# Optimization experiments

Hardware: AMD Instinct MI355X
Metric: run time of the kernel (lower is better)

Reference implementation:

```python
import jax, jax.numpy as jnp
import numpy as np

SPACE = 63
STRIDE = 2
TEMP = 0.07
W_CHAR, W_WORD, W_PHRASE, W_IDEA = 1.0, 0.5, 0.1, 0.1


def setup_inputs() -> dict:
    key = jax.random.key(0)
    ks = jax.random.split(key, 6)
    B, S, V, D = 8, 4096, 256, 512
    return {
        "logits": jax.random.normal(ks[0], (B, S, V), jnp.float32),
        "word_preds": jax.random.normal(ks[1], (B, D, S // STRIDE), jnp.float32),
        "char_features": jax.random.normal(ks[2], (B, D, S), jnp.float32),
        "contrastive_2": jax.random.normal(ks[3], (B, 128, 1024), jnp.float32),
        "contrastive_3": jax.random.normal(ks[4], (B, 128, 256), jnp.float32),
        "targets": jax.random.randint(ks[5], (B, S), 0, V, jnp.int32),
        "mask": jnp.ones((B, S), jnp.float32),
    }


def _info_nce(emb, temp=TEMP):
    # emb: (B, dim, L). Anchors = even positions, positives = odd positions.
    B, dim, L = emb.shape
    n_pairs = L // 2
    a = emb[:, :, 0:2 * n_pairs:2].transpose(0, 2, 1).reshape(-1, dim)
    p = emb[:, :, 1:2 * n_pairs:2].transpose(0, 2, 1).reshape(-1, dim)
    a = a / jnp.maximum(jnp.linalg.norm(a, axis=1, keepdims=True), 1e-12)
    p = p / jnp.maximum(jnp.linalg.norm(p, axis=1, keepdims=True), 1e-12)
    logits = (a @ p.T) / temp  # (n, n)
    n = logits.shape[0]
    logp = jax.nn.log_softmax(logits, axis=1)
    idx = jnp.arange(n)
    return -jnp.mean(logp[idx, idx])


def _word_span_loss(word_preds, char_features, targets, stride=STRIDE):
    # Segment-mean over spans between consecutive spaces; MSE vs gathered preds.
    B, D, S = char_features.shape
    Wlen = word_preds.shape[2]
    nseg = S + 2  # segment k in [1, n_spaces-1] = span after the k-th space; last slot = junk
    space = targets == SPACE
    cs = jnp.cumsum(space.astype(jnp.int32), axis=1)  # inclusive space count
    seg = jnp.where(space, nseg - 1, cs)          # non-space chars -> span id
    seg_sp = jnp.where(space, cs, nseg - 1)       # space positions -> their space index k
    t_idx = jnp.arange(S, dtype=jnp.int32)

    def per_batch(feats, seg_b, seg_sp_b):
        sums = jax.ops.segment_sum(feats.T, seg_b, num_segments=nseg)  # (nseg, D)
        cnts = jax.ops.segment_sum(jnp.ones((S,), feats.dtype), seg_b, num_segments=nseg)
        pos = jnp.full((nseg,), S, jnp.int32).at[seg_sp_b].set(t_idx)  # position of k-th space
        return sums, cnts, pos

    sums, cnts, pos = jax.vmap(per_batch)(char_features, seg, seg_sp)
    n_sp = cs[:, -1]  # (B,)
    k = jnp.arange(nseg)[None, :]
    valid = (k >= 1) & (k <= n_sp[:, None] - 1) & (cnts > 0) & ((pos // stride) < Wlen)
    means = jax.lax.stop_gradient(sums / jnp.maximum(cnts, 1.0)[..., None])  # target.detach()
    wp = jnp.clip(pos // stride, 0, Wlen - 1)  # (B, nseg)
    preds = jnp.take_along_axis(word_preds.transpose(0, 2, 1), wp[:, :, None], axis=1)  # (B,nseg,D)
    mse = jnp.mean((preds - means) ** 2, axis=-1)  # per-span F.mse_loss (mean over feat dim)
    tot = jnp.sum(jnp.where(valid, mse, 0.0))
    cnt = jnp.sum(valid).astype(mse.dtype)
    return jnp.where(cnt > 0, tot / jnp.maximum(cnt, 1.0), 0.0)


def reference(logits, word_preds, char_features, contrastive_2, contrastive_3, targets, mask):
    # char CE with mask
    logp = jax.nn.log_softmax(logits, axis=-1)
    ce = -jnp.take_along_axis(logp, targets[..., None].astype(jnp.int32), axis=-1)[..., 0]
    n = jnp.sum(mask)
    char_loss = jnp.where(n > 0, jnp.sum(ce * mask) / jnp.maximum(n, 1.0), jnp.mean(ce))
    word_loss = _word_span_loss(word_preds, char_features, targets)
    phrase_loss = _info_nce(contrastive_2)
    idea_loss = _info_nce(contrastive_3)
    return (W_CHAR * char_loss + W_WORD * word_loss
            + W_PHRASE * phrase_loss + W_IDEA * idea_loss)
```

## Files before the change

### kernel.cpp

```cpp
#include <hip/hip_runtime.h>

#define SPACE_TOK 63
#define INV_T 14.285714285714286f
#define SA_SCALE 20.609929155556595f
#define LN2F 0.6931471805599453f

typedef __attribute__((ext_vector_type(8))) short bf16x8;
typedef __attribute__((ext_vector_type(4))) float f32x4;

#define O_CECM   0
#define O_CEM    4096
#define O_CEC    8192
#define O_WPART  12288
#define O_WCNT   14336
#define O_PEXP2  14464
#define O_DIAG2  145536
#define O_PEXP3  161920
#define O_DIAG3  194688
#define O_A2     198848
#define SZ_A2    (4096*128*2)
#define O_P2     (O_A2 + SZ_A2)
#define O_A3     (O_P2 + SZ_A2)
#define SZ_A3    (1024*128*2)
#define O_P3     (O_A3 + SZ_A3)

#define SMEM_A 18048
#define SMEM_B 5632

__device__ inline unsigned short f2bf(float x) {
  union { float f; unsigned int u; } c; c.f = x;
  unsigned int r = c.u + 0x7fffu + ((c.u >> 16) & 1u);
  return (unsigned short)(r >> 16);
}

__device__ void norm_body(char* smem, const float* __restrict__ emb, int L,
                          unsigned short* __restrict__ Abf, unsigned short* __restrict__ Pbf,
                          int b, int l0) {
  float (*tile)[33] = (float(*)[33])smem;
  float (*np8)[32]  = (float(*)[32])(smem + 16896);
  float* scl        = (float*)(smem + 16896 + 1024);
  int tid = threadIdx.x;
  int lx = tid & 31, cq = tid >> 5;
  const float* eb = emb + (size_t)b * 128 * L + l0;
  for (int c = cq; c < 128; c += 8) tile[c][lx] = eb[(size_t)c * L + lx];
  __syncthreads();
  {
    float s = 0.f;
    for (int c = cq; c < 128; c += 8) { float x = tile[c][lx]; s += x * x; }
    np8[cq][lx] = s;
  }
  __syncthreads();
  if (tid < 32) {
    float t = 0.f;
#pragma unroll
    for (int g = 0; g < 8; ++g) t += np8[g][tid];
    float nrm = fmaxf(sqrtf(t), 1e-12f);
    scl[tid] = ((tid & 1) ? 1.0f : SA_SCALE) / nrm;
  }
  __syncthreads();
  int c = tid & 127, lh = tid >> 7;
  int half = L >> 1;
  int k = c >> 5, quad = (c >> 3) & 3, j = c & 7;
  for (int lp = lh; lp < 32; lp += 2) {
    int l = l0 + lp;
    int row = b * half + (l >> 1);
    unsigned short v = f2bf(tile[c][lp] * scl[lp]);
    unsigned short* dst = (l & 1) ? Pbf : Abf;
    dst[(size_t)(row >> 4) * 2048 + k * 512 + ((quad << 4) + (row & 15)) * 8 + j] = v;
  }
}

__global__ void __launch_bounds__(256) fusedA_kernel(const float* __restrict__ c2,
                                                     const float* __restrict__ c3,
                                                     char* __restrict__ ws) {
  extern __shared__ char smem[];
  int bid = blockIdx.x;
  if (bid < 256) {
    norm_body(smem, c2, 1024, (unsigned short*)(ws + O_A2), (unsigned short*)(ws + O_P2),
              bid & 7, (bid >> 3) * 32);
  } else {
    int nb = bid - 256;
    norm_body(smem, c3, 256, (unsigned short*)(ws + O_A3), (unsigned short*)(ws + O_P3),
              nb & 7, (nb >> 3) * 32);
  }
}

__device__ void word_body(char* smem, const float* __restrict__ wp,
                          const float* __restrict__ cf,
                          const int* __restrict__ targets,
                          char* __restrict__ ws, int w) {
  int* sc      = (int*)smem;
  int* splist  = (int*)(smem + 1024);
  int* snext_sh = (int*)(smem + 5120);
  float* wacc  = (float*)(smem + 5124);
  int tid = threadIdx.x;
  int z = w & 15, tq = (w >> 4) & 3, b = w >> 6;
  const int* tb = targets + b * 4096;
  int tbase = tq * 1024;
  int4 tok = ((const int4*)(tb + tbase))[tid];
  int f0 = (tok.x == SPACE_TOK), f1 = (tok.y == SPACE_TOK),
      f2 = (tok.z == SPACE_TOK), f3 = (tok.w == SPACE_TOK);
  int cnt = f0 + f1 + f2 + f3;
  sc[tid] = cnt;
  __syncthreads();
  for (int off = 1; off < 256; off <<= 1) {
    int v = (tid >= off) ? sc[tid - off] : 0;
    __syncthreads();
    sc[tid] += v;
    __syncthreads();
  }
  int base = sc[tid] - cnt;
  int p = tbase + tid * 4;
  if (f0) splist[base++] = p;
  if (f1) splist[base++] = p + 1;
  if (f2) splist[base++] = p + 2;
  if (f3) splist[base++] = p + 3;
  int m = sc[255];
  if (tid == 0) *snext_sh = -1;
  __syncthreads();
  if (m > 0) {
    for (int wstart = tbase + 1024; wstart < 4096 && *snext_sh < 0; wstart += 1024) {
      int t = wstart + tid * 4;
      int4 tk = ((const int4*)tb)[t >> 2];
      int found = 0x7fffffff;
      if (tk.x == SPACE_TOK) found = t;
      else if (tk.y == SPACE_TOK) found = t + 1;
      else if (tk.z == SPACE_TOK) found = t + 2;
      else if (tk.w == SPACE_TOK) found = t + 3;
#pragma unroll
      for (int mm = 1; mm < 64; mm <<= 1) found = min(found, __shfl_xor(found, mm));
      if ((tid & 63) == 0) sc[tid >> 6] = found;
      __syncthreads();
      if (tid == 0) {
        int f = min(min(sc[0], sc[1]), min(sc[2], sc[3]));
        if (f != 0x7fffffff) *snext_sh = f;
      }
      __syncthreads();
    }
  }
  int snext = *snext_sh;
  int wave = tid >> 6, lane = tid & 63;
  int dbase = z * 32 + wave * 8;
  const float* r0 = cf + ((size_t)(b * 512 + dbase)) * 4096;
  float myacc = 0.f;
  float lcnt = 0.f;
  for (int i = 0; i < m; ++i) {
    int t0 = splist[i];
    int t1 = (i + 1 < m) ? splist[i + 1] : snext;
    if (t1 < 0) break;
    int seglen = t1 - t0 - 1;
    if (seglen <= 0) continue;
    lcnt += 1.0f;
    int wpos = t0 >> 1;
    float invc = 1.0f / (float)seglen;
    int c0 = (t0 + 1) >> 2;
    int c1 = (t1 + 3) >> 2;
    float s0 = 0.f, s1 = 0.f, s2 = 0.f, s3 = 0.f, s4 = 0.f, s5 = 0.f, s6 = 0.f, s7 = 0.f;
    for (int c = c0 + lane; c < c1; c += 64) {
      int tbp = c << 2;
      float4 v0 = *(const float4*)(r0 + 0 * 4096 + tbp);
      float4 v1 = *(const float4*)(r0 + 1 * 4096 + tbp);
      float4 v2 = *(const float4*)(r0 + 2 * 4096 + tbp);
      float4 v3 = *(const float4*)(r0 + 3 * 4096 + tbp);
      float4 v4 = *(const float4*)(r0 + 4 * 4096 + tbp);
      float4 v5 = *(const float4*)(r0 + 5 * 4096 + tbp);
      float4 v6 = *(const float4*)(r0 + 6 * 4096 + tbp);
      float4 v7 = *(const float4*)(r0 + 7 * 4096 + tbp);
      float m0 = (tbp + 0 > t0 && tbp + 0 < t1) ? 1.f : 0.f;
      float m1 = (tbp + 1 > t0 && tbp + 1 < t1) ? 1.f : 0.f;
      float m2 = (tbp + 2 > t0 && tbp + 2 < t1) ? 1.f : 0.f;
      float m3 = (tbp + 3 > t0 && tbp + 3 < t1) ? 1.f : 0.f;
      s0 += v0.x * m0 + v0.y * m1 + v0.z * m2 + v0.w * m3;
      s1 += v1.x * m0 + v1.y * m1 + v1.z * m2 + v1.w * m3;
      s2 += v2.x * m0 + v2.y * m1 + v2.z * m2 + v2.w * m3;
      s3 += v3.x * m0 + v3.y * m1 + v3.z * m2 + v3.w * m3;
      s4 += v4.x * m0 + v4.y * m1 + v4.z * m2 + v4.w * m3;
      s5 += v5.x * m0 + v5.y * m1 + v5.z * m2 + v5.w * m3;
      s6 += v6.x * m0 + v6.y * m1 + v6.z * m2 + v6.w * m3;
      s7 += v7.x * m0 + v7.y * m1 + v7.z * m2 + v7.w * m3;
    }
#pragma unroll
    for (int mm = 1; mm < 64; mm <<= 1) {
      s0 += __shfl_xor(s0, mm); s1 += __shfl_xor(s1, mm);
      s2 += __shfl_xor(s2, mm); s3 += __shfl_xor(s3, mm);
      s4 += __shfl_xor(s4, mm); s5 += __shfl_xor(s5, mm);
      s6 += __shfl_xor(s6, mm); s7 += __shfl_xor(s7, mm);
    }
    if (lane < 8) {
      float sv = (lane == 0) ? s0 : (lane == 1) ? s1 : (lane == 2) ? s2 : (lane == 3) ? s3
               : (lane == 4) ? s4 : (lane == 5) ? s5 : (lane == 6) ? s6 : s7;
      float mean = sv * invc;
      float pred = wp[((size_t)(b * 512 + dbase + lane)) * 2048 + wpos];
      float diff = pred - mean;
      myacc += diff * diff;
    }
  }
#pragma unroll
  for (int mm = 1; mm < 8; mm <<= 1) myacc += __shfl_xor(myacc, mm);
  if (lane == 0) wacc[wave] = myacc;
  __syncthreads();
  if (tid == 0) {
    ((float*)(ws + O_WPART))[w] = (wacc[0] + wacc[1] + wacc[2] + wacc[3]) * (1.0f / 512.0f);
    if (z == 0) ((float*)(ws + O_WCNT))[w >> 4] = lcnt;
  }
}

__device__ void nce_body(char* smem, const unsigned short* __restrict__ A,
                         const unsigned short* __restrict__ P, int n, int sliceJ,
                         int blk_i, int s, float* __restrict__ pexp,
                         float* __restrict__ diag) {
  int tid = threadIdx.x;
  int wave = tid >> 6, lane = tid & 63;
  int col = lane & 15, quad = lane >> 4;
  int I0 = blk_i * 16;
  const unsigned short* At = A + (size_t)blk_i * 2048 + lane * 8;
  bf16x8 a0 = *(const bf16x8*)(At);
  bf16x8 a1 = *(const bf16x8*)(At + 512);
  bf16x8 a2 = *(const bf16x8*)(At + 1024);
  bf16x8 a3 = *(const bf16x8*)(At + 1536);
  float rl0 = 0.f, rl1 = 0.f, rl2 = 0.f, rl3 = 0.f;
  float dcap = 0.f;
  int perW = sliceJ >> 2;
  int J0w = s * sliceJ + wave * perW, Jend = J0w + perW;
#pragma unroll 2
  for (int J = J0w; J < Jend; J += 16) {
    const unsigned short* Pt = P + (size_t)(J >> 4) * 2048 + lane * 8;
    bf16x8 b0 = *(const bf16x8*)(Pt);
    bf16x8 b1 = *(const bf16x8*)(Pt + 512);
    bf16x8 b2 = *(const bf16x8*)(Pt + 1024);
    bf16x8 b3 = *(const bf16x8*)(Pt + 1536);
    f32x4 cfr = {0.f, 0.f, 0.f, 0.f};
    cfr = __builtin_amdgcn_mfma_f32_16x16x32_bf16(a0, b0, cfr, 0, 0, 0);
    cfr = __builtin_amdgcn_mfma_f32_16x16x32_bf16(a1, b1, cfr, 0, 0, 0);
    cfr = __builtin_amdgcn_mfma_f32_16x16x32_bf16(a2, b2, cfr, 0, 0, 0);
    cfr = __builtin_amdgcn_mfma_f32_16x16x32_bf16(a3, b3, cfr, 0, 0, 0);
    rl0 += exp2f(cfr[0] - SA_SCALE);
    rl1 += exp2f(cfr[1] - SA_SCALE);
    rl2 += exp2f(cfr[2] - SA_SCALE);
    rl3 += exp2f(cfr[3] - SA_SCALE);
    if (J == I0) {
      int r = col - (quad << 2);
      if (r == 0) dcap = cfr[0];
      else if (r == 1) dcap = cfr[1];
      else if (r == 2) dcap = cfr[2];
      else if (r == 3) dcap = cfr[3];
    }
  }
  float (*part)[16][17] = (float(*)[16][17])smem;
  float (*dpart)[16]    = (float(*)[16])(smem + 4352);
  part[wave][(quad << 2) + 0][col] = rl0;
  part[wave][(quad << 2) + 1][col] = rl1;
  part[wave][(quad << 2) + 2][col] = rl2;
  part[wave][(quad << 2) + 3][col] = rl3;
  if (quad == (col >> 2)) dpart[wave][col] = dcap;
  __syncthreads();
  {
    int rrow = tid >> 4, cc = tid & 15;
    float sv = 0.f, d = 0.f;
#pragma unroll
    for (int ww = 0; ww < 4; ++ww) { sv += part[ww][rrow][cc]; d += dpart[ww][rrow]; }
#pragma unroll
    for (int mm = 1; mm < 16; mm <<= 1) sv += __shfl_xor(sv, mm);
    if (cc == 0) {
      pexp[I0 + rrow] = sv;
      if (I0 >= s * sliceJ && I0 < (s + 1) * sliceJ) diag[I0 + rrow] = d;
    }
  }
}

__device__ void ce_body(char* smem, const float* __restrict__ logits,
                        const int* __restrict__ targets, const float* __restrict__ mask,
                        char* ws, int cb) {
  int tid = threadIdx.x;
  int wave = tid >> 6, lane = tid & 63;
  int rbase = cb * 32 + wave * 8;
  float4 v[8];
  float mk[8];
  int tg[8];
#pragma unroll
  for (int rr = 0; rr < 8; ++rr) v[rr] = ((const float4*)logits)[(size_t)(rbase + rr) * 64 + lane];
#pragma unroll
  for (int rr = 0; rr < 8; ++rr) { tg[rr] = targets[rbase + rr]; mk[rr] = mask[rbase + rr]; }
  float aCM = 0.f, aM = 0.f, aC = 0.f;
#pragma unroll
  for (int rr = 0; rr < 8; ++rr) {
    float e = __expf(v[rr].x) + __expf(v[rr].y) + __expf(v[rr].z) + __expf(v[rr].w);
#pragma unroll
    for (int m = 1; m < 64; m <<= 1) e += __shfl_xor(e, m);
    int t = tg[rr];
    int q = t & 3;
    float sel = (q == 0) ? v[rr].x : (q == 1) ? v[rr].y : (q == 2) ? v[rr].z : v[rr].w;
    float xt = __shfl(sel, t >> 2);
    float ce = __logf(e) - xt;
    aCM += ce * mk[rr]; aM += mk[rr]; aC += ce;
  }
  float (*red)[3] = (float(*)[3])smem;
  if (lane == 0) { red[wave][0] = aCM; red[wave][1] = aM; red[wave][2] = aC; }
  __syncthreads();
  if (tid == 0) {
    ((float*)(ws + O_CECM))[cb] = red[0][0] + red[1][0] + red[2][0] + red[3][0];
    ((float*)(ws + O_CEM ))[cb] = red[0][1] + red[1][1] + red[2][1] + red[3][1];
    ((float*)(ws + O_CEC ))[cb] = red[0][2] + red[1][2] + red[2][2] + red[3][2];
  }
}

__global__ void __launch_bounds__(256) fusedB_kernel(const float* __restrict__ logits,
                                                     const float* __restrict__ wp,
                                                     const float* __restrict__ cf,
                                                     const int* __restrict__ targets,
                                                     const float* __restrict__ mask,
                                                     char* __restrict__ ws) {
  extern __shared__ char smem[];
  int bid = blockIdx.x;
  if (bid < 512) {
    word_body(smem, wp, cf, targets, ws, bid);
  } else if (bid < 2560) {
    int nb = bid - 512;
    nce_body(smem, (const unsigned short*)(ws + O_A2), (const unsigned short*)(ws + O_P2),
             4096, 512, nb >> 3, nb & 7,
             (float*)(ws + O_PEXP2) + (nb & 7) * 4096, (float*)(ws + O_DIAG2));
  } else if (bid < 3072) {
    int nb = bid - 2560;
    nce_body(smem, (const unsigned short*)(ws + O_A3), (const unsigned short*)(ws + O_P3),
             1024, 128, nb >> 3, nb & 7,
             (float*)(ws + O_PEXP3) + (nb & 7) * 1024, (float*)(ws + O_DIAG3));
  } else {
    ce_body(smem, logits, targets, mask, ws, bid - 3072);
  }
}

__global__ void __launch_bounds__(256) final_kernel(const char* __restrict__ ws,
                                                    float* __restrict__ out) {
  int tid = threadIdx.x;
  int wave = tid >> 6, lane = tid & 63;
  float v[7] = {0.f, 0.f, 0.f, 0.f, 0.f, 0.f, 0.f};
  {
    float4 a = ((const float4*)(ws + O_CECM))[tid];
    float4 bb = ((const float4*)(ws + O_CEM))[tid];
    float4 c = ((const float4*)(ws + O_CEC))[tid];
    v[0] = a.x + a.y + a.z + a.w;
    v[1] = bb.x + bb.y + bb.z + bb.w;
    v[2] = c.x + c.y + c.z + c.w;
  }
  if (tid < 128) {
    float4 wv = ((const float4*)(ws + O_WPART))[tid];
    v[3] = wv.x + wv.y + wv.z + wv.w;
  }
  if (tid < 32) v[4] = ((const float*)(ws + O_WCNT))[tid];
  for (int r4 = tid; r4 < 1024; r4 += 256) {
    float4 S = {0.f, 0.f, 0.f, 0.f};
#pragma unroll
    for (int s = 0; s < 8; ++s) {
      float4 pv = ((const float4*)(ws + O_PEXP2))[s * 1024 + r4];
      S.x += pv.x; S.y += pv.y; S.z += pv.z; S.w += pv.w;
    }
    float4 dg = ((const float4*)(ws + O_DIAG2))[r4];
    v[5] += 4.0f * INV_T + __logf(S.x) + __logf(S.y) + __logf(S.z) + __logf(S.w)
            - LN2F * (dg.x + dg.y + dg.z + dg.w);
  }
  {
    int r4 = tid;
    float4 S = {0.f, 0.f, 0.f, 0.f};
#pragma unroll
    for (int s = 0; s < 8; ++s) {
      float4 pv = ((const float4*)(ws + O_PEXP3))[s * 256 + r4];
      S.x += pv.x; S.y += pv.y; S.z += pv.z; S.w += pv.w;
    }
    float4 dg = ((const float4*)(ws + O_DIAG3))[r4];
    v[6] = 4.0f * INV_T + __logf(S.x) + __logf(S.y) + __logf(S.z) + __logf(S.w)
           - LN2F * (dg.x + dg.y + dg.z + dg.w);
  }
#pragma unroll
  for (int j = 0; j < 7; ++j) {
    float x = v[j];
#pragma unroll
    for (int mm = 1; mm < 64; mm <<= 1) x += __shfl_xor(x, mm);
    v[j] = x;
  }
  __shared__ float fr[4][7];
  if (lane == 0)
#pragma unroll
    for (int j = 0; j < 7; ++j) fr[wave][j] = v[j];
  __syncthreads();
  if (tid == 0) {
    float s[7];
#pragma unroll
    for (int j = 0; j < 7; ++j) s[j] = fr[0][j] + fr[1][j] + fr[2][j] + fr[3][j];
    float n = s[1];
    float charL = (n > 0.f) ? (s[0] / fmaxf(n, 1.f)) : (s[2] / 32768.0f);
    float wordL = (s[4] > 0.f) ? (s[3] / fmaxf(s[4], 1.f)) : 0.f;
    out[0] = charL + 0.5f * wordL + 0.1f * (s[5] / 4096.0f) + 0.1f * (s[6] / 1024.0f);
  }
}

extern "C" void kernel_launch(void* const* d_in, const int* in_sizes, int n_in,
                              void* d_out, int out_size, void* d_ws, size_t ws_size,
                              hipStream_t stream) {
  (void)in_sizes; (void)n_in; (void)out_size; (void)ws_size;
  const float* logits        = (const float*)d_in[0];
  const float* word_preds    = (const float*)d_in[1];
  const float* char_features = (const float*)d_in[2];
  const float* c2            = (const float*)d_in[3];
  const float* c3            = (const float*)d_in[4];
  const int*   targets       = (const int*)d_in[5];
  const float* mask          = (const float*)d_in[6];
  float* out = (float*)d_out;
  char* ws = (char*)d_ws;

  fusedA_kernel<<<320, 256, SMEM_A, stream>>>(c2, c3, ws);
  fusedB_kernel<<<4096, 256, SMEM_B, stream>>>(logits, word_preds, char_features,
                                               targets, mask, ws);
  final_kernel<<<1, 256, 0, stream>>>(ws, out);
}
```

Measured before the change: 174.0 us.

## Merge three launches into one kernel with atomic work-stealing and last-block reduction

Replaces the three separate launches (normalize, fused losses, final reduce) with a single kernel plus a memset of the counters. NCE blocks, now scheduled after the word and CE blocks, pull the normalization tasks through an atomic counter and then spin until all of them finish. The last block to finish, detected with an atomic ticket, runs the final reduction. This removes launch gaps and lets the CE/word work overlap the normalization. In exchange it adds spin-waiting and raises shared memory per block for every block, which could lower occupancy for the CE blocks.

```diff
diff --git a/kernel.cpp b/kernel.cpp
--- a/kernel.cpp
+++ b/kernel.cpp
@@ -23,9 +23,12 @@
 #define O_A3     (O_P2 + SZ_A2)
 #define SZ_A3    (1024*128*2)
 #define O_P3     (O_A3 + SZ_A3)
-
-#define SMEM_A 18048
-#define SMEM_B 5632
+#define O_CTR    (O_P3 + SZ_A3)
+
+#define N_NORM_TASKS 320
+#define NBLK 4096
+
+#define SMEM_ALL 18048
 
 __device__ inline unsigned short f2bf(float x) {
   union { float f; unsigned int u; } c; c.f = x;
@@ -67,21 +70,6 @@
     unsigned short v = f2bf(tile[c][lp] * scl[lp]);
     unsigned short* dst = (l & 1) ? Pbf : Abf;
     dst[(size_t)(row >> 4) * 2048 + k * 512 + ((quad << 4) + (row & 15)) * 8 + j] = v;
-  }
-}
-
-__global__ void __launch_bounds__(256) fusedA_kernel(const float* __restrict__ c2,
-                                                     const float* __restrict__ c3,
-                                                     char* __restrict__ ws) {
-  extern __shared__ char smem[];
-  int bid = blockIdx.x;
-  if (bid < 256) {
-    norm_body(smem, c2, 1024, (unsigned short*)(ws + O_A2), (unsigned short*)(ws + O_P2),
-              bid & 7, (bid >> 3) * 32);
-  } else {
-    int nb = bid - 256;
-    norm_body(smem, c3, 256, (unsigned short*)(ws + O_A3), (unsigned short*)(ws + O_P3),
-              nb & 7, (nb >> 3) * 32);
   }
 }
 
@@ -304,33 +292,7 @@
   }
 }
 
-__global__ void __launch_bounds__(256) fusedB_kernel(const float* __restrict__ logits,
-                                                     const float* __restrict__ wp,
-                                                     const float* __restrict__ cf,
-                                                     const int* __restrict__ targets,
-                                                     const float* __restrict__ mask,
-                                                     char* __restrict__ ws) {
-  extern __shared__ char smem[];
-  int bid = blockIdx.x;
-  if (bid < 512) {
-    word_body(smem, wp, cf, targets, ws, bid);
-  } else if (bid < 2560) {
-    int nb = bid - 512;
-    nce_body(smem, (const unsigned short*)(ws + O_A2), (const unsigned short*)(ws + O_P2),
-             4096, 512, nb >> 3, nb & 7,
-             (float*)(ws + O_PEXP2) + (nb & 7) * 4096, (float*)(ws + O_DIAG2));
-  } else if (bid < 3072) {
-    int nb = bid - 2560;
-    nce_body(smem, (const unsigned short*)(ws + O_A3), (const unsigned short*)(ws + O_P3),
-             1024, 128, nb >> 3, nb & 7,
-             (float*)(ws + O_PEXP3) + (nb & 7) * 1024, (float*)(ws + O_DIAG3));
-  } else {
-    ce_body(smem, logits, targets, mask, ws, bid - 3072);
-  }
-}
-
-__global__ void __launch_bounds__(256) final_kernel(const char* __restrict__ ws,
-                                                    float* __restrict__ out) {
+__device__ void final_body(const char* __restrict__ ws, float* __restrict__ out) {
   int tid = threadIdx.x;
   int wave = tid >> 6, lane = tid & 63;
   float v[7] = {0.f, 0.f, 0.f, 0.f, 0.f, 0.f, 0.f};
@@ -390,6 +352,77 @@
     float charL = (n > 0.f) ? (s[0] / fmaxf(n, 1.f)) : (s[2] / 32768.0f);
     float wordL = (s[4] > 0.f) ? (s[3] / fmaxf(s[4], 1.f)) : 0.f;
     out[0] = charL + 0.5f * wordL + 0.1f * (s[5] / 4096.0f) + 0.1f * (s[6] / 1024.0f);
+  }
+}
+
+__global__ void __launch_bounds__(256) fused_all(const float* __restrict__ logits,
+                                                 const float* __restrict__ wp,
+                                                 const float* __restrict__ cf,
+                                                 const int* __restrict__ targets,
+                                                 const float* __restrict__ mask,
+                                                 const float* __restrict__ c2,
+                                                 const float* __restrict__ c3,
+                                                 char* __restrict__ ws,
+                                                 float* __restrict__ out) {
+  extern __shared__ char smem[];
+  __shared__ int s_flag;
+  unsigned* ctr = (unsigned*)(ws + O_CTR);
+  int bid = blockIdx.x;
+  int tid = threadIdx.x;
+
+  if (bid >= 1536) {
+    for (;;) {
+      if (tid == 0) {
+        unsigned d = __hip_atomic_load(&ctr[1], __ATOMIC_RELAXED, __HIP_MEMORY_SCOPE_AGENT);
+        s_flag = (d >= (unsigned)N_NORM_TASKS) ? 0x7fffffff : (int)atomicAdd(&ctr[0], 1u);
+      }
+      __syncthreads();
+      int t = s_flag;
+      if (t >= N_NORM_TASKS) break;
+      if (t < 256)
+        norm_body(smem, c2, 1024, (unsigned short*)(ws + O_A2), (unsigned short*)(ws + O_P2),
+                  t & 7, (t >> 3) * 32);
+      else {
+        int q = t - 256;
+        norm_body(smem, c3, 256, (unsigned short*)(ws + O_A3), (unsigned short*)(ws + O_P3),
+                  q & 7, (q >> 3) * 32);
+      }
+      __syncthreads();
+      if (tid == 0) { __threadfence(); atomicAdd(&ctr[1], 1u); }
+      __syncthreads();
+    }
+    if (tid == 0) {
+      while (__hip_atomic_load(&ctr[1], __ATOMIC_RELAXED, __HIP_MEMORY_SCOPE_AGENT)
+             < (unsigned)N_NORM_TASKS)
+        __builtin_amdgcn_s_sleep(8);
+      __threadfence();
+    }
+    __syncthreads();
+  }
+
+  if (bid < 512) {
+    word_body(smem, wp, cf, targets, ws, bid);
+  } else if (bid < 1536) {
+    ce_body(smem, logits, targets, mask, ws, bid - 512);
+  } else if (bid < 3584) {
+    int nb = bid - 1536;
+    nce_body(smem, (const unsigned short*)(ws + O_A2), (const unsigned short*)(ws + O_P2),
+             4096, 512, nb >> 3, nb & 7,
+             (float*)(ws + O_PEXP2) + (nb & 7) * 4096, (float*)(ws + O_DIAG2));
+  } else {
+    int nb = bid - 3584;
+    nce_body(smem, (const unsigned short*)(ws + O_A3), (const unsigned short*)(ws + O_P3),
+             1024, 128, nb >> 3, nb & 7,
+             (float*)(ws + O_PEXP3) + (nb & 7) * 1024, (float*)(ws + O_DIAG3));
+  }
+
+  __syncthreads();
+  if (tid == 0) { __threadfence(); s_flag = (int)atomicAdd(&ctr[2], 1u); }
+  __syncthreads();
+  if (s_flag == NBLK - 1) {
+    if (tid == 0) __threadfence();
+    __syncthreads();
+    final_body(ws, out);
   }
 }
 
@@ -407,8 +440,7 @@
   float* out = (float*)d_out;
   char* ws = (char*)d_ws;
 
-  fusedA_kernel<<<320, 256, SMEM_A, stream>>>(c2, c3, ws);
-  fusedB_kernel<<<4096, 256, SMEM_B, stream>>>(logits, word_preds, char_features,
-                                               targets, mask, ws);
-  final_kernel<<<1, 256, 0, stream>>>(ws, out);
-}
+  hipMemsetAsync(ws + O_CTR, 0, 64, stream);
+  fused_all<<<NBLK, 256, SMEM_ALL, stream>>>(logits, word_preds, char_features,
+                                             targets, mask, c2, c3, ws, out);
+}
```

New measurement: 548.2 us. +215.1%, slower.

## Split fused heterogeneous kernel into separate kernels and precompute space lists

Applied to the files above, without the earlier changes.

Moves the per-quarter space scan into the first kernel, which now writes compact 16-bit space-position lists and counts to workspace. It then splits the big heterogeneous fused kernel into separate NCE, CE and word-span kernels with their own shared-memory sizes. The word kernel hoists the prediction load ahead of the feature reduction. This removes the redundant scan that 16 word blocks each repeated and lets each kernel use tighter resources, at the cost of extra launches and no overlap between the stages. Space lists are capped at 512 entries per quarter, which silently truncates inputs with more spaces.

```diff
diff --git a/kernel.cpp b/kernel.cpp
--- a/kernel.cpp
+++ b/kernel.cpp
@@ -23,9 +23,15 @@
 #define O_A3     (O_P2 + SZ_A2)
 #define SZ_A3    (1024*128*2)
 #define O_P3     (O_A3 + SZ_A3)
+#define O_SEGM   (O_P3 + SZ_A3)
+#define O_SEGN   (O_SEGM + 128)
+#define O_SEGL   (O_SEGN + 128)
+#define SEG_CAP  512
 
 #define SMEM_A 18048
-#define SMEM_B 5632
+#define SMEM_N 4608
+#define SMEM_C 64
+#define SMEM_W 32
 
 __device__ inline unsigned short f2bf(float x) {
   union { float f; unsigned int u; } c; c.f = x;
@@ -70,31 +76,12 @@
   }
 }
 
-__global__ void __launch_bounds__(256) fusedA_kernel(const float* __restrict__ c2,
-                                                     const float* __restrict__ c3,
-                                                     char* __restrict__ ws) {
-  extern __shared__ char smem[];
-  int bid = blockIdx.x;
-  if (bid < 256) {
-    norm_body(smem, c2, 1024, (unsigned short*)(ws + O_A2), (unsigned short*)(ws + O_P2),
-              bid & 7, (bid >> 3) * 32);
-  } else {
-    int nb = bid - 256;
-    norm_body(smem, c3, 256, (unsigned short*)(ws + O_A3), (unsigned short*)(ws + O_P3),
-              nb & 7, (nb >> 3) * 32);
-  }
-}
-
-__device__ void word_body(char* smem, const float* __restrict__ wp,
-                          const float* __restrict__ cf,
-                          const int* __restrict__ targets,
-                          char* __restrict__ ws, int w) {
-  int* sc      = (int*)smem;
-  int* splist  = (int*)(smem + 1024);
-  int* snext_sh = (int*)(smem + 5120);
-  float* wacc  = (float*)(smem + 5124);
-  int tid = threadIdx.x;
-  int z = w & 15, tq = (w >> 4) & 3, b = w >> 6;
+__device__ void scan_body(char* smem, const int* __restrict__ targets,
+                          char* __restrict__ ws, int s) {
+  int* sc       = (int*)smem;
+  int* snext_sh = (int*)(smem + 1024);
+  int tid = threadIdx.x;
+  int b = s >> 2, tq = s & 3;
   const int* tb = targets + b * 4096;
   int tbase = tq * 1024;
   int4 tok = ((const int4*)(tb + tbase))[tid];
@@ -111,10 +98,11 @@
   }
   int base = sc[tid] - cnt;
   int p = tbase + tid * 4;
-  if (f0) splist[base++] = p;
-  if (f1) splist[base++] = p + 1;
-  if (f2) splist[base++] = p + 2;
-  if (f3) splist[base++] = p + 3;
+  unsigned short* segl = (unsigned short*)(ws + O_SEGL) + s * SEG_CAP;
+  if (f0) { if (base < SEG_CAP) segl[base] = (unsigned short)p;       base++; }
+  if (f1) { if (base < SEG_CAP) segl[base] = (unsigned short)(p + 1); base++; }
+  if (f2) { if (base < SEG_CAP) segl[base] = (unsigned short)(p + 2); base++; }
+  if (f3) { if (base < SEG_CAP) segl[base] = (unsigned short)(p + 3); base++; }
   int m = sc[255];
   if (tid == 0) *snext_sh = -1;
   __syncthreads();
@@ -138,21 +126,57 @@
       __syncthreads();
     }
   }
-  int snext = *snext_sh;
+  if (tid == 0) {
+    ((int*)(ws + O_SEGM))[s] = min(m, SEG_CAP);
+    ((int*)(ws + O_SEGN))[s] = *snext_sh;
+  }
+}
+
+__global__ void __launch_bounds__(256) fusedA_kernel(const float* __restrict__ c2,
+                                                     const float* __restrict__ c3,
+                                                     const int* __restrict__ targets,
+                                                     char* __restrict__ ws) {
+  extern __shared__ char smem[];
+  int bid = blockIdx.x;
+  if (bid < 256) {
+    norm_body(smem, c2, 1024, (unsigned short*)(ws + O_A2), (unsigned short*)(ws + O_P2),
+              bid & 7, (bid >> 3) * 32);
+  } else if (bid < 320) {
+    int nb = bid - 256;
+    norm_body(smem, c3, 256, (unsigned short*)(ws + O_A3), (unsigned short*)(ws + O_P3),
+              nb & 7, (nb >> 3) * 32);
+  } else {
+    scan_body(smem, targets, ws, bid - 320);
+  }
+}
+
+__global__ void __launch_bounds__(256) word_kernel(const float* __restrict__ wp,
+                                                   const float* __restrict__ cf,
+                                                   char* __restrict__ ws) {
+  __shared__ float wacc[4];
+  int tid = threadIdx.x;
+  int w = blockIdx.x;
+  int z = w & 15, tq = (w >> 4) & 3, b = w >> 6;
+  int s = b * 4 + tq;
+  int m     = ((const int*)(ws + O_SEGM))[s];
+  int snext = ((const int*)(ws + O_SEGN))[s];
+  const unsigned short* segl = (const unsigned short*)(ws + O_SEGL) + s * SEG_CAP;
   int wave = tid >> 6, lane = tid & 63;
   int dbase = z * 32 + wave * 8;
   const float* r0 = cf + ((size_t)(b * 512 + dbase)) * 4096;
   float myacc = 0.f;
   float lcnt = 0.f;
   for (int i = 0; i < m; ++i) {
-    int t0 = splist[i];
-    int t1 = (i + 1 < m) ? splist[i + 1] : snext;
+    int t0 = segl[i];
+    int t1 = (i + 1 < m) ? (int)segl[i + 1] : snext;
     if (t1 < 0) break;
     int seglen = t1 - t0 - 1;
     if (seglen <= 0) continue;
     lcnt += 1.0f;
     int wpos = t0 >> 1;
     float invc = 1.0f / (float)seglen;
+    float pred = 0.f;
+    if (lane < 8) pred = wp[((size_t)(b * 512 + dbase + lane)) * 2048 + wpos];
     int c0 = (t0 + 1) >> 2;
     int c1 = (t1 + 3) >> 2;
     float s0 = 0.f, s1 = 0.f, s2 = 0.f, s3 = 0.f, s4 = 0.f, s5 = 0.f, s6 = 0.f, s7 = 0.f;
@@ -190,7 +214,6 @@
       float sv = (lane == 0) ? s0 : (lane == 1) ? s1 : (lane == 2) ? s2 : (lane == 3) ? s3
                : (lane == 4) ? s4 : (lane == 5) ? s5 : (lane == 6) ? s6 : s7;
       float mean = sv * invc;
-      float pred = wp[((size_t)(b * 512 + dbase + lane)) * 2048 + wpos];
       float diff = pred - mean;
       myacc += diff * diff;
     }
@@ -268,10 +291,28 @@
   }
 }
 
-__device__ void ce_body(char* smem, const float* __restrict__ logits,
-                        const int* __restrict__ targets, const float* __restrict__ mask,
-                        char* ws, int cb) {
-  int tid = threadIdx.x;
+__global__ void __launch_bounds__(256) nce_kernel(char* __restrict__ ws) {
+  extern __shared__ char smem[];
+  int bid = blockIdx.x;
+  if (bid < 2048) {
+    nce_body(smem, (const unsigned short*)(ws + O_A2), (const unsigned short*)(ws + O_P2),
+             4096, 512, bid >> 3, bid & 7,
+             (float*)(ws + O_PEXP2) + (bid & 7) * 4096, (float*)(ws + O_DIAG2));
+  } else {
+    int nb = bid - 2048;
+    nce_body(smem, (const unsigned short*)(ws + O_A3), (const unsigned short*)(ws + O_P3),
+             1024, 128, nb >> 3, nb & 7,
+             (float*)(ws + O_PEXP3) + (nb & 7) * 1024, (float*)(ws + O_DIAG3));
+  }
+}
+
+__global__ void __launch_bounds__(256) ce_kernel(const float* __restrict__ logits,
+                                                 const int* __restrict__ targets,
+                                                 const float* __restrict__ mask,
+                                                 char* __restrict__ ws) {
+  __shared__ float red[4][3];
+  int tid = threadIdx.x;
+  int cb = blockIdx.x;
   int wave = tid >> 6, lane = tid & 63;
   int rbase = cb * 32 + wave * 8;
   float4 v[8];
@@ -294,38 +335,12 @@
     float ce = __logf(e) - xt;
     aCM += ce * mk[rr]; aM += mk[rr]; aC += ce;
   }
-  float (*red)[3] = (float(*)[3])smem;
   if (lane == 0) { red[wave][0] = aCM; red[wave][1] = aM; red[wave][2] = aC; }
   __syncthreads();
   if (tid == 0) {
     ((float*)(ws + O_CECM))[cb] = red[0][0] + red[1][0] + red[2][0] + red[3][0];
     ((float*)(ws + O_CEM ))[cb] = red[0][1] + red[1][1] + red[2][1] + red[3][1];
     ((float*)(ws + O_CEC ))[cb] = red[0][2] + red[1][2] + red[2][2] + red[3][2];
-  }
-}
-
-__global__ void __launch_bounds__(256) fusedB_kernel(const float* __restrict__ logits,
-                                                     const float* __restrict__ wp,
-                                                     const float* __restrict__ cf,
-                                                     const int* __restrict__ targets,
-                                                     const float* __restrict__ mask,
-                                                     char* __restrict__ ws) {
-  extern __shared__ char smem[];
-  int bid = blockIdx.x;
-  if (bid < 512) {
-    word_body(smem, wp, cf, targets, ws, bid);
-  } else if (bid < 2560) {
-    int nb = bid - 512;
-    nce_body(smem, (const unsigned short*)(ws + O_A2), (const unsigned short*)(ws + O_P2),
-             4096, 512, nb >> 3, nb & 7,
-             (float*)(ws + O_PEXP2) + (nb & 7) * 4096, (float*)(ws + O_DIAG2));
-  } else if (bid < 3072) {
-    int nb = bid - 2560;
-    nce_body(smem, (const unsigned short*)(ws + O_A3), (const unsigned short*)(ws + O_P3),
-             1024, 128, nb >> 3, nb & 7,
-             (float*)(ws + O_PEXP3) + (nb & 7) * 1024, (float*)(ws + O_DIAG3));
-  } else {
-    ce_body(smem, logits, targets, mask, ws, bid - 3072);
   }
 }
 
@@ -407,8 +422,9 @@
   float* out = (float*)d_out;
   char* ws = (char*)d_ws;
 
-  fusedA_kernel<<<320, 256, SMEM_A, stream>>>(c2, c3, ws);
-  fusedB_kernel<<<4096, 256, SMEM_B, stream>>>(logits, word_preds, char_features,
-                                               targets, mask, ws);
+  fusedA_kernel<<<352, 256, SMEM_A, stream>>>(c2, c3, targets, ws);
+  nce_kernel<<<2560, 256, SMEM_N, stream>>>(ws);
+  ce_kernel<<<1024, 256, SMEM_C, stream>>>(logits, targets, mask, ws);
+  word_kernel<<<512, 256, SMEM_W, stream>>>(word_preds, char_features, ws);
   final_kernel<<<1, 256, 0, stream>>>(ws, out);
 }
```

After: 188.8 us. 1.09x slower.

## Regroup kernels and tile InfoNCE over four row blocks per workgroup

Applied to the files above, without the earlier changes.

Moves the memory-bound word-span, cross-entropy and normalization work into one first kernel, and runs the InfoNCE matmul in a separate second kernel. Each InfoNCE workgroup now keeps four 16-row A tiles in registers, so every loaded P tile feeds four MFMA chains and P loads per FLOP drop to a quarter. The word-span body also issues its prediction load before the reduction loop to hide latency. In exchange, register pressure and LDS use per workgroup go up, the InfoNCE launch has fewer blocks, and the bandwidth-bound work no longer overlaps the matmul inside one launch.

```diff
diff --git a/kernel.cpp b/kernel.cpp
--- a/kernel.cpp
+++ b/kernel.cpp
@@ -24,8 +24,9 @@
 #define SZ_A3    (1024*128*2)
 #define O_P3     (O_A3 + SZ_A3)
 
-#define SMEM_A 18048
-#define SMEM_B 5632
+#define SMEM_A   18048
+#define NTILE    4
+#define SMEM_NCE (4*64*17*4 + 4*64*4)
 
 __device__ inline unsigned short f2bf(float x) {
   union { float f; unsigned int u; } c; c.f = x;
@@ -67,21 +68,6 @@
     unsigned short v = f2bf(tile[c][lp] * scl[lp]);
     unsigned short* dst = (l & 1) ? Pbf : Abf;
     dst[(size_t)(row >> 4) * 2048 + k * 512 + ((quad << 4) + (row & 15)) * 8 + j] = v;
-  }
-}
-
-__global__ void __launch_bounds__(256) fusedA_kernel(const float* __restrict__ c2,
-                                                     const float* __restrict__ c3,
-                                                     char* __restrict__ ws) {
-  extern __shared__ char smem[];
-  int bid = blockIdx.x;
-  if (bid < 256) {
-    norm_body(smem, c2, 1024, (unsigned short*)(ws + O_A2), (unsigned short*)(ws + O_P2),
-              bid & 7, (bid >> 3) * 32);
-  } else {
-    int nb = bid - 256;
-    norm_body(smem, c3, 256, (unsigned short*)(ws + O_A3), (unsigned short*)(ws + O_P3),
-              nb & 7, (nb >> 3) * 32);
   }
 }
 
@@ -153,6 +139,8 @@
     lcnt += 1.0f;
     int wpos = t0 >> 1;
     float invc = 1.0f / (float)seglen;
+    float pred = 0.f;
+    if (lane < 8) pred = wp[((size_t)(b * 512 + dbase + lane)) * 2048 + wpos];
     int c0 = (t0 + 1) >> 2;
     int c1 = (t1 + 3) >> 2;
     float s0 = 0.f, s1 = 0.f, s2 = 0.f, s3 = 0.f, s4 = 0.f, s5 = 0.f, s6 = 0.f, s7 = 0.f;
@@ -190,7 +178,6 @@
       float sv = (lane == 0) ? s0 : (lane == 1) ? s1 : (lane == 2) ? s2 : (lane == 3) ? s3
                : (lane == 4) ? s4 : (lane == 5) ? s5 : (lane == 6) ? s6 : s7;
       float mean = sv * invc;
-      float pred = wp[((size_t)(b * 512 + dbase + lane)) * 2048 + wpos];
       float diff = pred - mean;
       myacc += diff * diff;
     }
@@ -202,69 +189,6 @@
   if (tid == 0) {
     ((float*)(ws + O_WPART))[w] = (wacc[0] + wacc[1] + wacc[2] + wacc[3]) * (1.0f / 512.0f);
     if (z == 0) ((float*)(ws + O_WCNT))[w >> 4] = lcnt;
-  }
-}
-
-__device__ void nce_body(char* smem, const unsigned short* __restrict__ A,
-                         const unsigned short* __restrict__ P, int n, int sliceJ,
-                         int blk_i, int s, float* __restrict__ pexp,
-                         float* __restrict__ diag) {
-  int tid = threadIdx.x;
-  int wave = tid >> 6, lane = tid & 63;
-  int col = lane & 15, quad = lane >> 4;
-  int I0 = blk_i * 16;
-  const unsigned short* At = A + (size_t)blk_i * 2048 + lane * 8;
-  bf16x8 a0 = *(const bf16x8*)(At);
-  bf16x8 a1 = *(const bf16x8*)(At + 512);
-  bf16x8 a2 = *(const bf16x8*)(At + 1024);
-  bf16x8 a3 = *(const bf16x8*)(At + 1536);
-  float rl0 = 0.f, rl1 = 0.f, rl2 = 0.f, rl3 = 0.f;
-  float dcap = 0.f;
-  int perW = sliceJ >> 2;
-  int J0w = s * sliceJ + wave * perW, Jend = J0w + perW;
-#pragma unroll 2
-  for (int J = J0w; J < Jend; J += 16) {
-    const unsigned short* Pt = P + (size_t)(J >> 4) * 2048 + lane * 8;
-    bf16x8 b0 = *(const bf16x8*)(Pt);
-    bf16x8 b1 = *(const bf16x8*)(Pt + 512);
-    bf16x8 b2 = *(const bf16x8*)(Pt + 1024);
-    bf16x8 b3 = *(const bf16x8*)(Pt + 1536);
-    f32x4 cfr = {0.f, 0.f, 0.f, 0.f};
-    cfr = __builtin_amdgcn_mfma_f32_16x16x32_bf16(a0, b0, cfr, 0, 0, 0);
-    cfr = __builtin_amdgcn_mfma_f32_16x16x32_bf16(a1, b1, cfr, 0, 0, 0);
-    cfr = __builtin_amdgcn_mfma_f32_16x16x32_bf16(a2, b2, cfr, 0, 0, 0);
-    cfr = __builtin_amdgcn_mfma_f32_16x16x32_bf16(a3, b3, cfr, 0, 0, 0);
-    rl0 += exp2f(cfr[0] - SA_SCALE);
-    rl1 += exp2f(cfr[1] - SA_SCALE);
-    rl2 += exp2f(cfr[2] - SA_SCALE);
-    rl3 += exp2f(cfr[3] - SA_SCALE);
-    if (J == I0) {
-      int r = col - (quad << 2);
-      if (r == 0) dcap = cfr[0];
-      else if (r == 1) dcap = cfr[1];
-      else if (r == 2) dcap = cfr[2];
-      else if (r == 3) dcap = cfr[3];
-    }
-  }
-  float (*part)[16][17] = (float(*)[16][17])smem;
-  float (*dpart)[16]    = (float(*)[16])(smem + 4352);
-  part[wave][(quad << 2) + 0][col] = rl0;
-  part[wave][(quad << 2) + 1][col] = rl1;
-  part[wave][(quad << 2) + 2][col] = rl2;
-  part[wave][(quad << 2) + 3][col] = rl3;
-  if (quad == (col >> 2)) dpart[wave][col] = dcap;
-  __syncthreads();
-  {
-    int rrow = tid >> 4, cc = tid & 15;
-    float sv = 0.f, d = 0.f;
-#pragma unroll
-    for (int ww = 0; ww < 4; ++ww) { sv += part[ww][rrow][cc]; d += dpart[ww][rrow]; }
-#pragma unroll
-    for (int mm = 1; mm < 16; mm <<= 1) sv += __shfl_xor(sv, mm);
-    if (cc == 0) {
-      pexp[I0 + rrow] = sv;
-      if (I0 >= s * sliceJ && I0 < (s + 1) * sliceJ) diag[I0 + rrow] = d;
-    }
   }
 }
 
@@ -304,28 +228,124 @@
   }
 }
 
-__global__ void __launch_bounds__(256) fusedB_kernel(const float* __restrict__ logits,
+__global__ void __launch_bounds__(256) fusedA_kernel(const float* __restrict__ logits,
                                                      const float* __restrict__ wp,
                                                      const float* __restrict__ cf,
                                                      const int* __restrict__ targets,
                                                      const float* __restrict__ mask,
+                                                     const float* __restrict__ c2,
+                                                     const float* __restrict__ c3,
                                                      char* __restrict__ ws) {
   extern __shared__ char smem[];
   int bid = blockIdx.x;
   if (bid < 512) {
     word_body(smem, wp, cf, targets, ws, bid);
-  } else if (bid < 2560) {
+  } else if (bid < 1536) {
+    ce_body(smem, logits, targets, mask, ws, bid - 512);
+  } else if (bid < 1792) {
+    int nb = bid - 1536;
+    norm_body(smem, c2, 1024, (unsigned short*)(ws + O_A2), (unsigned short*)(ws + O_P2),
+              nb & 7, (nb >> 3) * 32);
+  } else {
+    int nb = bid - 1792;
+    norm_body(smem, c3, 256, (unsigned short*)(ws + O_A3), (unsigned short*)(ws + O_P3),
+              nb & 7, (nb >> 3) * 32);
+  }
+}
+
+__device__ void nce_body(char* smem, const unsigned short* __restrict__ A,
+                         const unsigned short* __restrict__ P, int sliceJ,
+                         int grp, int s, float* __restrict__ pexp,
+                         float* __restrict__ diag) {
+  int tid = threadIdx.x;
+  int wave = tid >> 6, lane = tid & 63;
+  int col = lane & 15, quad = lane >> 4;
+  int I0g = grp * (16 * NTILE);
+  const unsigned short* At = A + (size_t)(I0g >> 4) * 2048 + lane * 8;
+  bf16x8 a[NTILE][4];
+#pragma unroll
+  for (int t = 0; t < NTILE; ++t)
+#pragma unroll
+    for (int k = 0; k < 4; ++k)
+      a[t][k] = *(const bf16x8*)(At + t * 2048 + k * 512);
+  float rl[NTILE][4];
+#pragma unroll
+  for (int t = 0; t < NTILE; ++t)
+#pragma unroll
+    for (int q = 0; q < 4; ++q) rl[t][q] = 0.f;
+  float dcap[NTILE];
+#pragma unroll
+  for (int t = 0; t < NTILE; ++t) dcap[t] = 0.f;
+  int perW = sliceJ >> 2;
+  int J0w = s * sliceJ + wave * perW, Jend = J0w + perW;
+  for (int J = J0w; J < Jend; J += 16) {
+    const unsigned short* Pt = P + (size_t)(J >> 4) * 2048 + lane * 8;
+    bf16x8 b0 = *(const bf16x8*)(Pt);
+    bf16x8 b1 = *(const bf16x8*)(Pt + 512);
+    bf16x8 b2 = *(const bf16x8*)(Pt + 1024);
+    bf16x8 b3 = *(const bf16x8*)(Pt + 1536);
+#pragma unroll
+    for (int t = 0; t < NTILE; ++t) {
+      f32x4 cfr = {0.f, 0.f, 0.f, 0.f};
+      cfr = __builtin_amdgcn_mfma_f32_16x16x32_bf16(a[t][0], b0, cfr, 0, 0, 0);
+      cfr = __builtin_amdgcn_mfma_f32_16x16x32_bf16(a[t][1], b1, cfr, 0, 0, 0);
+      cfr = __builtin_amdgcn_mfma_f32_16x16x32_bf16(a[t][2], b2, cfr, 0, 0, 0);
+      cfr = __builtin_amdgcn_mfma_f32_16x16x32_bf16(a[t][3], b3, cfr, 0, 0, 0);
+      rl[t][0] += exp2f(cfr[0] - SA_SCALE);
+      rl[t][1] += exp2f(cfr[1] - SA_SCALE);
+      rl[t][2] += exp2f(cfr[2] - SA_SCALE);
+      rl[t][3] += exp2f(cfr[3] - SA_SCALE);
+      if (J == I0g + 16 * t) {
+        int r = col - (quad << 2);
+        if (r == 0) dcap[t] = cfr[0];
+        else if (r == 1) dcap[t] = cfr[1];
+        else if (r == 2) dcap[t] = cfr[2];
+        else if (r == 3) dcap[t] = cfr[3];
+      }
+    }
+  }
+  float (*part)[64][17] = (float(*)[64][17])smem;
+  float (*dpart)[64]    = (float(*)[64])(smem + 18496);
+#pragma unroll
+  for (int t = 0; t < NTILE; ++t) {
+    part[wave][t * 16 + (quad << 2) + 0][col] = rl[t][0];
+    part[wave][t * 16 + (quad << 2) + 1][col] = rl[t][1];
+    part[wave][t * 16 + (quad << 2) + 2][col] = rl[t][2];
+    part[wave][t * 16 + (quad << 2) + 3][col] = rl[t][3];
+    if (quad == (col >> 2)) dpart[wave][t * 16 + col] = dcap[t];
+  }
+  __syncthreads();
+  {
+    int rrow = tid >> 4, cc = tid & 15;
+#pragma unroll
+    for (int t = 0; t < NTILE; ++t) {
+      int row = t * 16 + rrow;
+      float sv = 0.f, d = 0.f;
+#pragma unroll
+      for (int ww = 0; ww < 4; ++ww) { sv += part[ww][row][cc]; d += dpart[ww][row]; }
+#pragma unroll
+      for (int mm = 1; mm < 16; mm <<= 1) sv += __shfl_xor(sv, mm);
+      if (cc == 0) {
+        int gi = I0g + row;
+        pexp[gi] = sv;
+        if (gi >= s * sliceJ && gi < (s + 1) * sliceJ) diag[gi] = d;
+      }
+    }
+  }
+}
+
+__global__ void __launch_bounds__(256) nce_kernel(char* __restrict__ ws) {
+  extern __shared__ char smem[];
+  int bid = blockIdx.x;
+  if (bid < 512) {
+    nce_body(smem, (const unsigned short*)(ws + O_A2), (const unsigned short*)(ws + O_P2),
+             512, bid >> 3, bid & 7,
+             (float*)(ws + O_PEXP2) + (bid & 7) * 4096, (float*)(ws + O_DIAG2));
+  } else {
     int nb = bid - 512;
-    nce_body(smem, (const unsigned short*)(ws + O_A2), (const unsigned short*)(ws + O_P2),
-             4096, 512, nb >> 3, nb & 7,
-             (float*)(ws + O_PEXP2) + (nb & 7) * 4096, (float*)(ws + O_DIAG2));
-  } else if (bid < 3072) {
-    int nb = bid - 2560;
     nce_body(smem, (const unsigned short*)(ws + O_A3), (const unsigned short*)(ws + O_P3),
-             1024, 128, nb >> 3, nb & 7,
+             128, nb >> 3, nb & 7,
              (float*)(ws + O_PEXP3) + (nb & 7) * 1024, (float*)(ws + O_DIAG3));
-  } else {
-    ce_body(smem, logits, targets, mask, ws, bid - 3072);
   }
 }
 
@@ -407,8 +427,8 @@
   float* out = (float*)d_out;
   char* ws = (char*)d_ws;
 
-  fusedA_kernel<<<320, 256, SMEM_A, stream>>>(c2, c3, ws);
-  fusedB_kernel<<<4096, 256, SMEM_B, stream>>>(logits, word_preds, char_features,
-                                               targets, mask, ws);
+  fusedA_kernel<<<1856, 256, SMEM_A, stream>>>(logits, word_preds, char_features,
+                                               targets, mask, c2, c3, ws);
+  nce_kernel<<<640, 256, SMEM_NCE, stream>>>(ws);
   final_kernel<<<1, 256, 0, stream>>>(ws, out);
 }
```

Result: no change. 173.7 us, median of 2 (-0.1%).
